# Kernel optimization log

Hardware: AMD Instinct MI355X
Metric: run time of the kernel (lower is better)

## Reference

```python
import jax, jax.numpy as jnp
import numpy as np

N, E, D, H, EF = 50000, 800000, 64, 64, 16


def setup_inputs() -> dict:
    key = jax.random.key(0)
    ks = jax.random.split(key, 12)
    s = 0.05
    return {
        "node_feat": jax.random.normal(ks[0], (N, D), jnp.float32),
        "coord": jax.random.normal(ks[1], (N, 3), jnp.float32),
        "edge_feat": jax.random.normal(ks[2], (E, EF), jnp.float32),
        "src": jax.random.randint(ks[3], (E,), 0, N, jnp.int32),
        "dst": jax.random.randint(ks[4], (E,), 0, N, jnp.int32),
        "W_e1": jax.random.normal(ks[5], (2 * D + EF + 1, H), jnp.float32) * s,
        "b_e1": jnp.zeros((H,), jnp.float32),
        "W_e2": jax.random.normal(ks[6], (H, H), jnp.float32) * s,
        "b_e2": jnp.zeros((H,), jnp.float32),
        "W_n1": jax.random.normal(ks[7], (D + H, H), jnp.float32) * s,
        "b_n1": jnp.zeros((H,), jnp.float32),
        "W_n2": jax.random.normal(ks[8], (H, D), jnp.float32) * s,
        "b_n2": jnp.zeros((D,), jnp.float32),
    }


def reference(node_feat, coord, edge_feat, src, dst,
              W_e1, b_e1, W_e2, b_e2, W_n1, b_n1, W_n2, b_n2):
    # per-edge radial distance: ||coord_src - coord_dst||^2  -> [E,1]
    x_diff = coord[src] - coord[dst]
    radial = jnp.sum(x_diff * x_diff, axis=-1, keepdims=True)
    # edge message MLP: concat [h_src, h_dst, radial, a] -> SiLU MLP
    f = jnp.concatenate([node_feat[src], node_feat[dst], radial, edge_feat], axis=-1)
    m = jax.nn.silu(f @ W_e1 + b_e1)
    msg = jax.nn.silu(m @ W_e2 + b_e2)  # [E,H]
    # scatter-sum aggregation to destination nodes
    h_neigh = jax.ops.segment_sum(msg, dst, num_segments=node_feat.shape[0])
    # node update MLP
    z = jnp.concatenate([node_feat, h_neigh], axis=-1)
    h = jax.nn.silu(z @ W_n1 + b_n1) @ W_n2 + b_n2
    return h
```

## Files before the change

### kernel.cpp

```cpp
#include <hip/hip_runtime.h>

#define D 64
#define H 64
#define EFD 16
#define MS 68
#define TE 128
#define TN 128
#define DPB 16

__device__ __forceinline__ float silu(float x) {
    return x / (1.0f + __expf(-x));
}

#define GEMM_STEP(acc_, a_, bf_) do { \
    const float* bp_ = (const float*)(bf_); \
    acc_[0] += (a_).x*bp_[0] + (a_).y*bp_[4] + (a_).z*bp_[8]  + (a_).w*bp_[12]; \
    acc_[1] += (a_).x*bp_[1] + (a_).y*bp_[5] + (a_).z*bp_[9]  + (a_).w*bp_[13]; \
    acc_[2] += (a_).x*bp_[2] + (a_).y*bp_[6] + (a_).z*bp_[10] + (a_).w*bp_[14]; \
    acc_[3] += (a_).x*bp_[3] + (a_).y*bp_[7] + (a_).z*bp_[11] + (a_).w*bp_[15]; \
} while (0)

#define PGEMM64(acc_, Wp_, wrow0_, eg_, hg_, smem_) do { \
    for (int k4 = 0; k4 < 16; k4++) { \
        float4 bf_[4]; \
        _Pragma("unroll") \
        for (int kk = 0; kk < 4; kk++) \
            bf_[kk] = *(const float4*)&(Wp_)[(size_t)((wrow0_) + 4*k4 + kk) * H + 4*(hg_)]; \
        _Pragma("unroll") \
        for (int i = 0; i < 8; i++) { \
            float4 a_ = *(const float4*)&(smem_)[(8*(eg_) + i) * MS + 4*k4]; \
            GEMM_STEP(acc_[i], a_, bf_); \
        } \
    } \
} while (0)


__global__ __launch_bounds__(256) void hist_kernel(
    const int* __restrict__ dst, int* __restrict__ deg, int E)
{
    int e = blockIdx.x * 256 + threadIdx.x;
    if (e < E) atomicAdd(&deg[dst[e]], 1);
}

__global__ __launch_bounds__(1024, 1) void scan_kernel(
    const int* __restrict__ deg, int* __restrict__ cursor, int N)
{
    __shared__ int wsums[16];
    __shared__ int carry_s;
    const int tid = threadIdx.x;
    const int lane = tid & 63, wid = tid >> 6;
    if (tid == 0) carry_s = 0;
    __syncthreads();
    for (int base = 0; base < N; base += 1024) {
        int idx = base + tid;
        int v = (idx < N) ? deg[idx] : 0;
        int x = v;
        #pragma unroll
        for (int off = 1; off < 64; off <<= 1) {
            int y = __shfl_up(x, off, 64);
            if (lane >= off) x += y;
        }
        if (lane == 63) wsums[wid] = x;
        __syncthreads();
        if (wid == 0) {
            int ws = (lane < 16) ? wsums[lane] : 0;
            #pragma unroll
            for (int off = 1; off < 16; off <<= 1) {
                int y = __shfl_up(ws, off, 64);
                if (lane >= off) ws += y;
            }
            if (lane < 16) wsums[lane] = ws;
        }
        __syncthreads();
        int wprefix = (wid > 0) ? wsums[wid - 1] : 0;
        int excl = carry_s + wprefix + x - v;
        if (idx < N) cursor[idx] = excl;
        __syncthreads();
        if (tid == 0) carry_s += wsums[15];
        __syncthreads();
    }
}

__global__ __launch_bounds__(256) void build2_kernel(
    const int* __restrict__ dst, const int* __restrict__ src,
    int* __restrict__ cursor,
    int* __restrict__ eidx, int* __restrict__ srcs, int* __restrict__ dsts,
    int E)
{
    int e = blockIdx.x * 256 + threadIdx.x;
    if (e < E) {
        int d2 = dst[e];
        int pos = atomicAdd(&cursor[d2], 1);
        eidx[pos] = e;
        srcs[pos] = src[e];
        dsts[pos] = d2;
    }
}

__global__ __launch_bounds__(256) void build_kernel(
    const int* __restrict__ dst, int* __restrict__ cursor,
    int* __restrict__ eidx, int E)
{
    int e = blockIdx.x * 256 + threadIdx.x;
    if (e < E) {
        int pos = atomicAdd(&cursor[dst[e]], 1);
        eidx[pos] = e;
    }
}


__global__ __launch_bounds__(256, 4) void pre_kernel(
    const float* __restrict__ node_feat,
    const float* __restrict__ W_e1, const float* __restrict__ b_e1,
    float* __restrict__ Pa, float* __restrict__ Pb, int N)
{
    __shared__ float smem[TN * MS];
    const int tid = threadIdx.x;
    const int nbase = blockIdx.x * TN;
    const int ng = tid >> 4, hg = tid & 15, k = tid & 63, no = tid >> 6;

    #pragma unroll
    for (int t = 0; t < 32; t++) {
        int gn = nbase + no + 4*t;
        int cg = (gn < N) ? gn : (N - 1);
        smem[(no + 4*t) * MS + k] = node_feat[(size_t)cg * D + k];
    }
    __syncthreads();

    float accA[8][4], accB[8][4];
    {
        float4 b0 = *(const float4*)&b_e1[4*hg];
        #pragma unroll
        for (int i = 0; i < 8; i++) {
            accA[i][0]=b0.x; accA[i][1]=b0.y; accA[i][2]=b0.z; accA[i][3]=b0.w;
            accB[i][0]=0.f;  accB[i][1]=0.f;  accB[i][2]=0.f;  accB[i][3]=0.f;
        }
    }
    PGEMM64(accA, W_e1, 0,  ng, hg, smem);
    PGEMM64(accB, W_e1, 64, ng, hg, smem);

    #pragma unroll
    for (int i = 0; i < 8; i++) {
        int gn = nbase + 8*ng + i;
        if (gn < N) {
            float4 a; a.x=accA[i][0]; a.y=accA[i][1]; a.z=accA[i][2]; a.w=accA[i][3];
            float4 b; b.x=accB[i][0]; b.y=accB[i][1]; b.z=accB[i][2]; b.w=accB[i][3];
            *(float4*)&Pa[(size_t)gn * H + 4*hg] = a;
            *(float4*)&Pb[(size_t)gn * H + 4*hg] = b;
        }
    }
}


__global__ __launch_bounds__(256, 4) void edge_kernel2(
    const float* __restrict__ Pa, const float* __restrict__ Pb,
    const float* __restrict__ coord,
    const float* __restrict__ edge_feat,
    const int* __restrict__ eidx, const int* __restrict__ srcs,
    const int* __restrict__ dsts,
    const int* __restrict__ cursor_end, const int* __restrict__ deg,
    const float* __restrict__ W_e1,
    const float* __restrict__ W_e2, const float* __restrict__ b_e2,
    float* __restrict__ h_neigh, int N)
{
    __shared__ float smem[TE * MS];
    __shared__ float hacc[DPB * H];
    __shared__ int ssrc[TE], sdlo[TE], seid[TE];

    const int tid = threadIdx.x;
    const int dst0 = blockIdx.x * DPB;
    const int dlast = min(dst0 + DPB, N) - 1;
    const int rs = cursor_end[dst0] - deg[dst0];
    const int re = cursor_end[dlast];

    for (int i = tid; i < DPB * H; i += 256) hacc[i] = 0.f;

    const int eg = tid >> 4;
    const int hg = tid & 15;

    for (int base = rs; base < re; base += TE) {
        const int cnt = min(re - base, TE);
        __syncthreads();

        if (tid < TE) {
            int e = 0, s = 0, dl = -1;
            float radial = 0.f;
            if (tid < cnt) {
                int p = base + tid;
                e = eidx[p]; s = srcs[p];
                int d2 = dsts[p]; dl = d2 - dst0;
                float dx = coord[s*3+0] - coord[d2*3+0];
                float dy = coord[s*3+1] - coord[d2*3+1];
                float dz = coord[s*3+2] - coord[d2*3+2];
                radial = dx*dx + dy*dy + dz*dz;
            }
            ssrc[tid] = s; sdlo[tid] = dl; seid[tid] = e;
            smem[tid * MS + 0] = radial;
        }
        __syncthreads();

        {
            const int k2 = tid & 15, e2 = tid >> 4;
            #pragma unroll
            for (int t = 0; t < 8; t++) {
                int r = e2 + 16*t;
                float v = (sdlo[r] >= 0) ? edge_feat[(size_t)seid[r] * EFD + k2] : 0.f;
                smem[r * MS + 1 + k2] = v;
            }
        }

        float acc[8][4];
        #pragma unroll
        for (int i = 0; i < 8; i++) {
            int r = 8*eg + i;
            int s = ssrc[r];
            int dl = sdlo[r];
            int drow = (dl >= 0) ? (dst0 + dl) : 0;
            float4 pa = *(const float4*)&Pa[(size_t)s * H + 4*hg];
            float4 pb = *(const float4*)&Pb[(size_t)drow * H + 4*hg];
            acc[i][0] = pa.x + pb.x; acc[i][1] = pa.y + pb.y;
            acc[i][2] = pa.z + pb.z; acc[i][3] = pa.w + pb.w;
        }
        __syncthreads();

        for (int k4 = 0; k4 < 4; k4++) {
            float4 bf[4];
            #pragma unroll
            for (int kk = 0; kk < 4; kk++)
                bf[kk] = *(const float4*)&W_e1[(size_t)(128 + 4*k4 + kk) * H + 4*hg];
            #pragma unroll
            for (int i = 0; i < 8; i++) {
                float4 a = *(const float4*)&smem[(8*eg + i) * MS + 4*k4];
                GEMM_STEP(acc[i], a, bf);
            }
        }
        {
            float4 b = *(const float4*)&W_e1[(size_t)144 * H + 4*hg];
            #pragma unroll
            for (int i = 0; i < 8; i++) {
                float a = smem[(8*eg+i)*MS + 16];
                acc[i][0] += a*b.x; acc[i][1] += a*b.y; acc[i][2] += a*b.z; acc[i][3] += a*b.w;
            }
        }
        __syncthreads();

        #pragma unroll
        for (int i = 0; i < 8; i++) {
            float4 mv;
            mv.x = silu(acc[i][0]); mv.y = silu(acc[i][1]);
            mv.z = silu(acc[i][2]); mv.w = silu(acc[i][3]);
            *(float4*)&smem[(8*eg+i)*MS + 4*hg] = mv;
        }
        __syncthreads();

        float acc2[8][4];
        {
            float4 b0 = *(const float4*)&b_e2[4*hg];
            #pragma unroll
            for (int i = 0; i < 8; i++) {
                acc2[i][0]=b0.x; acc2[i][1]=b0.y; acc2[i][2]=b0.z; acc2[i][3]=b0.w;
            }
        }
        PGEMM64(acc2, W_e2, 0, eg, hg, smem);

        float rx=0.f, ry=0.f, rz=0.f, rw=0.f;
        int cur = -1;
        #pragma unroll
        for (int i = 0; i < 8; i++) {
            int r = 8*eg + i;
            int dl = sdlo[r];
            if (dl < 0) continue;
            float vx = silu(acc2[i][0]), vy = silu(acc2[i][1]);
            float vz = silu(acc2[i][2]), vw = silu(acc2[i][3]);
            if (dl != cur) {
                if (cur >= 0) {
                    float* hp = &hacc[cur * H + 4*hg];
                    atomicAdd(&hp[0], rx); atomicAdd(&hp[1], ry);
                    atomicAdd(&hp[2], rz); atomicAdd(&hp[3], rw);
                }
                cur = dl; rx = vx; ry = vy; rz = vz; rw = vw;
            } else {
                rx += vx; ry += vy; rz += vz; rw += vw;
            }
        }
        if (cur >= 0) {
            float* hp = &hacc[cur * H + 4*hg];
            atomicAdd(&hp[0], rx); atomicAdd(&hp[1], ry);
            atomicAdd(&hp[2], rz); atomicAdd(&hp[3], rw);
        }
    }

    __syncthreads();
    {
        const int dloc = tid >> 4;
        const int ch = 4 * (tid & 15);
        int gd = dst0 + dloc;
        if (gd < N) {
            float4 v = *(const float4*)&hacc[dloc * H + ch];
            *(float4*)&h_neigh[(size_t)gd * H + ch] = v;
        }
    }
}


template <int MODE>
__global__ __launch_bounds__(256, 4) void edge_kernel(
    const float* __restrict__ node_feat,
    const float* __restrict__ coord,
    const float* __restrict__ edge_feat,
    const int* __restrict__ src,
    const int* __restrict__ dst,
    const int* __restrict__ eidx_g,
    const float* __restrict__ W_e1, const float* __restrict__ b_e1,
    const float* __restrict__ W_e2, const float* __restrict__ b_e2,
    float* __restrict__ h_neigh,
    int E)
{
    __shared__ float smem[TE * MS];
    __shared__ int ssrc[TE];
    __shared__ int sdst[TE];
    __shared__ int seid[TE];

    const int tid = threadIdx.x;
    const int ebase = blockIdx.x * TE;

    float radial = 0.f;
    if (tid < TE) {
        int p = ebase + tid;
        int e = p, s = 0, d2 = -1;
        if (p < E) {
            if (MODE == 1) e = eidx_g[p];
            s = src[e];
            d2 = dst[e];
        }
        ssrc[tid] = s;
        sdst[tid] = d2;
        seid[tid] = e;
        if (d2 >= 0) {
            float dx = coord[s*3+0] - coord[d2*3+0];
            float dy = coord[s*3+1] - coord[d2*3+1];
            float dz = coord[s*3+2] - coord[d2*3+2];
            radial = dx*dx + dy*dy + dz*dz;
        }
    }
    __syncthreads();

    const int eg = tid >> 4;
    const int hg = tid & 15;
    const int k  = tid & 63;
    const int eo = tid >> 6;

    float acc[8][4];
    {
        float4 b0 = *(const float4*)&b_e1[4*hg];
        #pragma unroll
        for (int i = 0; i < 8; i++) {
            acc[i][0]=b0.x; acc[i][1]=b0.y; acc[i][2]=b0.z; acc[i][3]=b0.w;
        }
    }

    float rA[32];
    #pragma unroll
    for (int t = 0; t < 32; t++)
        rA[t] = node_feat[(size_t)ssrc[eo + 4*t] * D + k];
    #pragma unroll
    for (int t = 0; t < 32; t++)
        smem[(eo + 4*t) * MS + k] = rA[t];
    __syncthreads();

    float rB[32];
    #pragma unroll
    for (int t = 0; t < 32; t++) {
        int row = sdst[eo + 4*t];
        row = row < 0 ? 0 : row;
        rB[t] = node_feat[(size_t)row * D + k];
    }
    PGEMM64(acc, W_e1, 0, eg, hg, smem);
    __syncthreads();

    #pragma unroll
    for (int t = 0; t < 32; t++)
        smem[(eo + 4*t) * MS + k] = rB[t];
    __syncthreads();

    float rC[8];
    {
        const int k2 = tid & 15, e2 = tid >> 4;
        #pragma unroll
        for (int t = 0; t < 8; t++) {
            int r = e2 + 16*t;
            rC[t] = (ebase + r < E) ? edge_feat[(size_t)seid[r] * EFD + k2] : 0.f;
        }
    }
    PGEMM64(acc, W_e1, 64, eg, hg, smem);
    __syncthreads();

    {
        const int k2 = tid & 15, e2 = tid >> 4;
        #pragma unroll
        for (int t = 0; t < 8; t++)
            smem[(e2 + 16*t) * MS + 1 + k2] = rC[t];
        if (tid < TE) smem[tid * MS + 0] = radial;
    }
    __syncthreads();

    for (int k4 = 0; k4 < 4; k4++) {
        float4 bf[4];
        #pragma unroll
        for (int kk = 0; kk < 4; kk++)
            bf[kk] = *(const float4*)&W_e1[(size_t)(128 + 4*k4 + kk) * H + 4*hg];
        #pragma unroll
        for (int i = 0; i < 8; i++) {
            float4 a = *(const float4*)&smem[(8*eg + i) * MS + 4*k4];
            GEMM_STEP(acc[i], a, bf);
        }
    }
    {
        float4 b = *(const float4*)&W_e1[(size_t)144 * H + 4*hg];
        #pragma unroll
        for (int i = 0; i < 8; i++) {
            float a = smem[(8*eg+i)*MS + 16];
            acc[i][0] += a*b.x; acc[i][1] += a*b.y; acc[i][2] += a*b.z; acc[i][3] += a*b.w;
        }
    }
    __syncthreads();

    #pragma unroll
    for (int i = 0; i < 8; i++) {
        float4 mv;
        mv.x = silu(acc[i][0]); mv.y = silu(acc[i][1]);
        mv.z = silu(acc[i][2]); mv.w = silu(acc[i][3]);
        *(float4*)&smem[(8*eg+i)*MS + 4*hg] = mv;
    }
    __syncthreads();

    float acc2[8][4];
    {
        float4 b0 = *(const float4*)&b_e2[4*hg];
        #pragma unroll
        for (int i = 0; i < 8; i++) {
            acc2[i][0]=b0.x; acc2[i][1]=b0.y; acc2[i][2]=b0.z; acc2[i][3]=b0.w;
        }
    }
    PGEMM64(acc2, W_e2, 0, eg, hg, smem);

    if (MODE == 0) {
        #pragma unroll
        for (int i = 0; i < 8; i++) {
            int r = 8*eg + i;
            int dr = sdst[r];
            if (dr >= 0) {
                float* hp = &h_neigh[(size_t)dr * H + 4*hg];
                atomicAdd(&hp[0], silu(acc2[i][0]));
                atomicAdd(&hp[1], silu(acc2[i][1]));
                atomicAdd(&hp[2], silu(acc2[i][2]));
                atomicAdd(&hp[3], silu(acc2[i][3]));
            }
        }
    } else {
        __syncthreads();
        #pragma unroll
        for (int i = 0; i < 8; i++) {
            float4 mv;
            mv.x = silu(acc2[i][0]); mv.y = silu(acc2[i][1]);
            mv.z = silu(acc2[i][2]); mv.w = silu(acc2[i][3]);
            *(float4*)&smem[(8*eg+i)*MS + 4*hg] = mv;
        }
        __syncthreads();

        int emaxt = E - ebase; if (emaxt > TE) emaxt = TE;
        #pragma unroll 1
        for (int i = 0; i < 8; i++) {
            int r = 8*eg + i;
            if (r >= emaxt) break;
            int dr = sdst[r];
            if (dr < 0) continue;
            if (r > 0 && sdst[r-1] == dr) continue;
            float4 s = *(const float4*)&smem[r*MS + 4*hg];
            int rr = r + 1;
            while (rr < emaxt && sdst[rr] == dr) {
                const float* mp = &smem[rr*MS + 4*hg];
                s.x += mp[0]; s.y += mp[1]; s.z += mp[2]; s.w += mp[3];
                rr++;
            }
            float* hp = &h_neigh[(size_t)dr * H + 4*hg];
            atomicAdd(&hp[0], s.x); atomicAdd(&hp[1], s.y);
            atomicAdd(&hp[2], s.z); atomicAdd(&hp[3], s.w);
        }
    }
}


__global__ __launch_bounds__(256, 4) void node_kernel(
    const float* __restrict__ node_feat,
    const float* __restrict__ h_neigh,
    const float* __restrict__ W_n1, const float* __restrict__ b_n1,
    const float* __restrict__ W_n2, const float* __restrict__ b_n2,
    float* __restrict__ out, int N)
{
    __shared__ float smem[TN * MS];

    const int tid = threadIdx.x;
    const int nbase = blockIdx.x * TN;

    const int ng = tid >> 4;
    const int hg = tid & 15;
    const int k  = tid & 63;
    const int no = tid >> 6;

    float acc[8][4];
    {
        float4 b0 = *(const float4*)&b_n1[4*hg];
        #pragma unroll
        for (int i = 0; i < 8; i++) {
            acc[i][0]=b0.x; acc[i][1]=b0.y; acc[i][2]=b0.z; acc[i][3]=b0.w;
        }
    }

    float rA[32];
    #pragma unroll
    for (int t = 0; t < 32; t++) {
        int gn = nbase + no + 4*t;
        int cg = (gn < N) ? gn : (N - 1);
        rA[t] = node_feat[(size_t)cg * D + k];
    }
    #pragma unroll
    for (int t = 0; t < 32; t++)
        smem[(no + 4*t) * MS + k] = rA[t];
    __syncthreads();

    float rB[32];
    #pragma unroll
    for (int t = 0; t < 32; t++) {
        int gn = nbase + no + 4*t;
        int cg = (gn < N) ? gn : (N - 1);
        rB[t] = h_neigh[(size_t)cg * H + k];
    }
    PGEMM64(acc, W_n1, 0, ng, hg, smem);
    __syncthreads();

    #pragma unroll
    for (int t = 0; t < 32; t++)
        smem[(no + 4*t) * MS + k] = rB[t];
    __syncthreads();

    PGEMM64(acc, W_n1, 64, ng, hg, smem);
    __syncthreads();

    #pragma unroll
    for (int i = 0; i < 8; i++) {
        float4 mv;
        mv.x = silu(acc[i][0]); mv.y = silu(acc[i][1]);
        mv.z = silu(acc[i][2]); mv.w = silu(acc[i][3]);
        *(float4*)&smem[(8*ng+i)*MS + 4*hg] = mv;
    }
    __syncthreads();

    float acc2[8][4];
    {
        float4 b0 = *(const float4*)&b_n2[4*hg];
        #pragma unroll
        for (int i = 0; i < 8; i++) {
            acc2[i][0]=b0.x; acc2[i][1]=b0.y; acc2[i][2]=b0.z; acc2[i][3]=b0.w;
        }
    }
    PGEMM64(acc2, W_n2, 0, ng, hg, smem);

    #pragma unroll
    for (int i = 0; i < 8; i++) {
        int gn = nbase + 8*ng + i;
        if (gn < N) {
            float4 ov;
            ov.x = acc2[i][0]; ov.y = acc2[i][1]; ov.z = acc2[i][2]; ov.w = acc2[i][3];
            *(float4*)&out[(size_t)gn * D + 4*hg] = ov;
        }
    }
}

extern "C" void kernel_launch(void* const* d_in, const int* in_sizes, int n_in,
                              void* d_out, int out_size, void* d_ws, size_t ws_size,
                              hipStream_t stream)
{
    const float* node_feat = (const float*)d_in[0];
    const float* coord     = (const float*)d_in[1];
    const float* edge_feat = (const float*)d_in[2];
    const int*   src       = (const int*)d_in[3];
    const int*   dst       = (const int*)d_in[4];
    const float* W_e1 = (const float*)d_in[5];
    const float* b_e1 = (const float*)d_in[6];
    const float* W_e2 = (const float*)d_in[7];
    const float* b_e2 = (const float*)d_in[8];
    const float* W_n1 = (const float*)d_in[9];
    const float* b_n1 = (const float*)d_in[10];
    const float* W_n2 = (const float*)d_in[11];
    const float* b_n2 = (const float*)d_in[12];

    const int N = in_sizes[0] / D;
    const int E = in_sizes[3];

    const size_t hn_b   = (size_t)N * H * sizeof(float);
    const size_t n_i    = (size_t)N * sizeof(int);
    const size_t e_i    = (size_t)E * sizeof(int);
    const size_t p_b    = (size_t)N * H * sizeof(float);

    const size_t need2 = hn_b + 2*n_i + 3*e_i + 2*p_b;
    const size_t need1 = hn_b + 2*n_i + e_i;

    float* h_neigh = (float*)d_ws;
    const int eblocks = (E + TE - 1) / TE;

    if (ws_size >= need2) {
        char* p = (char*)d_ws + hn_b;
        int* deg    = (int*)p;              p += n_i;
        int* cursor = (int*)p;              p += n_i;
        int* eidx   = (int*)p;              p += e_i;
        int* srcs   = (int*)p;              p += e_i;
        int* dsts   = (int*)p;              p += e_i;
        float* Pa   = (float*)p;            p += p_b;
        float* Pb   = (float*)p;

        hipMemsetAsync(deg, 0, n_i, stream);
        hist_kernel<<<(E + 255) / 256, 256, 0, stream>>>(dst, deg, E);
        scan_kernel<<<1, 1024, 0, stream>>>(deg, cursor, N);
        build2_kernel<<<(E + 255) / 256, 256, 0, stream>>>(dst, src, cursor,
                                                           eidx, srcs, dsts, E);
        pre_kernel<<<(N + TN - 1) / TN, 256, 0, stream>>>(node_feat, W_e1, b_e1,
                                                          Pa, Pb, N);
        const int dblocks = (N + DPB - 1) / DPB;
        edge_kernel2<<<dblocks, 256, 0, stream>>>(Pa, Pb, coord, edge_feat,
                                                  eidx, srcs, dsts, cursor, deg,
                                                  W_e1, W_e2, b_e2, h_neigh, N);
    } else if (ws_size >= need1) {
        int* deg    = (int*)((char*)d_ws + hn_b);
        int* cursor = (int*)((char*)deg + n_i);
        int* eidx   = (int*)((char*)cursor + n_i);
        hipMemsetAsync(d_ws, 0, hn_b + n_i, stream);
        hist_kernel<<<(E + 255) / 256, 256, 0, stream>>>(dst, deg, E);
        scan_kernel<<<1, 1024, 0, stream>>>(deg, cursor, N);
        build_kernel<<<(E + 255) / 256, 256, 0, stream>>>(dst, cursor, eidx, E);
        edge_kernel<1><<<eblocks, 256, 0, stream>>>(node_feat, coord, edge_feat,
                                                    src, dst, eidx,
                                                    W_e1, b_e1, W_e2, b_e2,
                                                    h_neigh, E);
    } else {
        hipMemsetAsync(d_ws, 0, hn_b, stream);
        edge_kernel<0><<<eblocks, 256, 0, stream>>>(node_feat, coord, edge_feat,
                                                    src, dst, nullptr,
                                                    W_e1, b_e1, W_e2, b_e2,
                                                    h_neigh, E);
    }

    const int nblocks = (N + TN - 1) / TN;
    node_kernel<<<nblocks, 256, 0, stream>>>(node_feat, h_neigh,
                                             W_n1, b_n1, W_n2, b_n2,
                                             (float*)d_out, N);
}
```

Baseline: 646.8 us.

## Parallelize degree scan, pre-sort edge features with radial, prefetch next edge tile

Replaces the single-block serial scan with a three-kernel block-partitioned scan (reduce, scan partials, apply). The build step now writes edge features and the precomputed radial into a CSR-ordered 20-float record per edge, so the edge kernel reads them contiguously instead of gathering through eidx and coord. The new edge kernel reads these records directly from global memory, and it issues the Pa/Pb gathers for the next tile before the second GEMM to overlap latency. The cost is an extra E*80-byte buffer written and read, a larger workspace requirement, and higher register pressure (occupancy hint lowered to 3).

```diff
diff --git a/kernel.cpp b/kernel.cpp
--- a/kernel.cpp
+++ b/kernel.cpp
@@ -7,6 +7,7 @@
 #define TE 128
 #define TN 128
 #define DPB 16
+#define REFW 20
 
 __device__ __forceinline__ float silu(float x) {
     return x / (1.0f + __expf(-x));
@@ -42,43 +43,96 @@
     if (e < E) atomicAdd(&deg[dst[e]], 1);
 }
 
-__global__ __launch_bounds__(1024, 1) void scan_kernel(
-    const int* __restrict__ deg, int* __restrict__ cursor, int N)
-{
-    __shared__ int wsums[16];
+
+__global__ __launch_bounds__(256) void scanA_kernel(
+    const int* __restrict__ deg, int* __restrict__ part, int N)
+{
+    __shared__ int tmp[256];
+    const int tid = threadIdx.x;
+    int idx = blockIdx.x * 256 + tid;
+    tmp[tid] = (idx < N) ? deg[idx] : 0;
+    __syncthreads();
+    for (int off = 128; off > 0; off >>= 1) {
+        if (tid < off) tmp[tid] += tmp[tid + off];
+        __syncthreads();
+    }
+    if (tid == 0) part[blockIdx.x] = tmp[0];
+}
+
+__global__ __launch_bounds__(256, 1) void scanB_kernel(
+    int* __restrict__ part, int nparts)
+{
+    __shared__ int tmp[256];
     __shared__ int carry_s;
     const int tid = threadIdx.x;
-    const int lane = tid & 63, wid = tid >> 6;
     if (tid == 0) carry_s = 0;
     __syncthreads();
-    for (int base = 0; base < N; base += 1024) {
+    for (int base = 0; base < nparts; base += 256) {
         int idx = base + tid;
-        int v = (idx < N) ? deg[idx] : 0;
-        int x = v;
-        #pragma unroll
-        for (int off = 1; off < 64; off <<= 1) {
-            int y = __shfl_up(x, off, 64);
-            if (lane >= off) x += y;
-        }
-        if (lane == 63) wsums[wid] = x;
-        __syncthreads();
-        if (wid == 0) {
-            int ws = (lane < 16) ? wsums[lane] : 0;
-            #pragma unroll
-            for (int off = 1; off < 16; off <<= 1) {
-                int y = __shfl_up(ws, off, 64);
-                if (lane >= off) ws += y;
-            }
-            if (lane < 16) wsums[lane] = ws;
-        }
-        __syncthreads();
-        int wprefix = (wid > 0) ? wsums[wid - 1] : 0;
-        int excl = carry_s + wprefix + x - v;
-        if (idx < N) cursor[idx] = excl;
-        __syncthreads();
-        if (tid == 0) carry_s += wsums[15];
-        __syncthreads();
-    }
+        int v = (idx < nparts) ? part[idx] : 0;
+        tmp[tid] = v;
+        __syncthreads();
+        #pragma unroll
+        for (int off = 1; off < 256; off <<= 1) {
+            int t = (tid >= off) ? tmp[tid - off] : 0;
+            __syncthreads();
+            tmp[tid] += t;
+            __syncthreads();
+        }
+        int incl = tmp[tid];
+        int tot = tmp[255];
+        if (idx < nparts) part[idx] = carry_s + incl - v;
+        __syncthreads();
+        if (tid == 0) carry_s += tot;
+        __syncthreads();
+    }
+}
+
+__global__ __launch_bounds__(256) void scanC_kernel(
+    const int* __restrict__ deg, const int* __restrict__ part,
+    int* __restrict__ cursor, int N)
+{
+    __shared__ int tmp[256];
+    const int tid = threadIdx.x;
+    int idx = blockIdx.x * 256 + tid;
+    int v = (idx < N) ? deg[idx] : 0;
+    tmp[tid] = v;
+    __syncthreads();
+    #pragma unroll
+    for (int off = 1; off < 256; off <<= 1) {
+        int t = (tid >= off) ? tmp[tid - off] : 0;
+        __syncthreads();
+        tmp[tid] += t;
+        __syncthreads();
+    }
+    if (idx < N) cursor[idx] = part[blockIdx.x] + tmp[tid] - v;
+}
+
+
+__global__ __launch_bounds__(256) void build3_kernel(
+    const int* __restrict__ dst, const int* __restrict__ src,
+    const float* __restrict__ coord, const float* __restrict__ edge_feat,
+    int* __restrict__ cursor,
+    int* __restrict__ srcs, int* __restrict__ dsts, float* __restrict__ refr,
+    int E)
+{
+    int e = blockIdx.x * 256 + threadIdx.x;
+    if (e >= E) return;
+    int d2 = dst[e];
+    int s = src[e];
+    int pos = atomicAdd(&cursor[d2], 1);
+    srcs[pos] = s;
+    dsts[pos] = d2;
+    float dx = coord[s*3+0] - coord[d2*3+0];
+    float dy = coord[s*3+1] - coord[d2*3+1];
+    float dz = coord[s*3+2] - coord[d2*3+2];
+    float* rr = &refr[(size_t)pos * REFW];
+    const float4* ef = (const float4*)&edge_feat[(size_t)e * EFD];
+    *(float4*)&rr[0]  = ef[0];
+    *(float4*)&rr[4]  = ef[1];
+    *(float4*)&rr[8]  = ef[2];
+    *(float4*)&rr[12] = ef[3];
+    rr[16] = dx*dx + dy*dy + dz*dz;
 }
 
 __global__ __launch_bounds__(256) void build2_kernel(
@@ -97,17 +151,6 @@
     }
 }
 
-__global__ __launch_bounds__(256) void build_kernel(
-    const int* __restrict__ dst, int* __restrict__ cursor,
-    int* __restrict__ eidx, int E)
-{
-    int e = blockIdx.x * 256 + threadIdx.x;
-    if (e < E) {
-        int pos = atomicAdd(&cursor[dst[e]], 1);
-        eidx[pos] = e;
-    }
-}
-
 
 __global__ __launch_bounds__(256, 4) void pre_kernel(
     const float* __restrict__ node_feat,
@@ -149,6 +192,147 @@
             *(float4*)&Pb[(size_t)gn * H + 4*hg] = b;
         }
     }
+}
+
+
+__global__ __launch_bounds__(256, 3) void edge_kernel3(
+    const float* __restrict__ Pa, const float* __restrict__ Pb,
+    const int* __restrict__ srcs, const int* __restrict__ dsts,
+    const float* __restrict__ refr,
+    const int* __restrict__ cursor_end, const int* __restrict__ deg,
+    const float* __restrict__ W_e1,
+    const float* __restrict__ W_e2, const float* __restrict__ b_e2,
+    float* __restrict__ h_neigh, int N)
+{
+    __shared__ float smem[TE * MS];
+    __shared__ float hacc[DPB * H];
+
+    const int tid = threadIdx.x;
+    const int dst0 = blockIdx.x * DPB;
+    const int dlast = min(dst0 + DPB, N) - 1;
+    const int rs = cursor_end[dst0] - deg[dst0];
+    const int re = cursor_end[dlast];
+
+    for (int i = tid; i < DPB * H; i += 256) hacc[i] = 0.f;
+
+    const int eg = tid >> 4, hg = tid & 15;
+
+    float acc[8][4];
+    int dl[8];
+
+    #define LOAD_TILE(base_, acc_, dl_) do { \
+        _Pragma("unroll") \
+        for (int i_ = 0; i_ < 8; i_++) { \
+            int p_ = (base_) + 8*eg + i_; \
+            bool val_ = (p_ < re); \
+            int pp_ = val_ ? p_ : (re - 1); \
+            int s_ = srcs[pp_]; \
+            int d2_ = dsts[pp_]; \
+            float4 pa_ = *(const float4*)&Pa[(size_t)s_ * H + 4*hg]; \
+            float4 pb_ = *(const float4*)&Pb[(size_t)d2_ * H + 4*hg]; \
+            acc_[i_][0] = pa_.x + pb_.x; acc_[i_][1] = pa_.y + pb_.y; \
+            acc_[i_][2] = pa_.z + pb_.z; acc_[i_][3] = pa_.w + pb_.w; \
+            dl_[i_] = val_ ? (d2_ - dst0) : -1; \
+        } \
+    } while (0)
+
+    if (re > rs) LOAD_TILE(rs, acc, dl);
+
+    for (int base = rs; base < re; base += TE) {
+        for (int k4 = 0; k4 < 4; k4++) {
+            float4 bf[4];
+            #pragma unroll
+            for (int kk = 0; kk < 4; kk++)
+                bf[kk] = *(const float4*)&W_e1[(size_t)(129 + 4*k4 + kk) * H + 4*hg];
+            #pragma unroll
+            for (int i = 0; i < 8; i++) {
+                int p = base + 8*eg + i;
+                int pp = (p < re) ? p : (re - 1);
+                float4 a = *(const float4*)&refr[(size_t)pp * REFW + 4*k4];
+                GEMM_STEP(acc[i], a, bf);
+            }
+        }
+        {
+            float4 b = *(const float4*)&W_e1[(size_t)128 * H + 4*hg];
+            #pragma unroll
+            for (int i = 0; i < 8; i++) {
+                int p = base + 8*eg + i;
+                int pp = (p < re) ? p : (re - 1);
+                float a = refr[(size_t)pp * REFW + 16];
+                acc[i][0] += a*b.x; acc[i][1] += a*b.y;
+                acc[i][2] += a*b.z; acc[i][3] += a*b.w;
+            }
+        }
+
+        #pragma unroll
+        for (int i = 0; i < 8; i++) {
+            float4 mv;
+            mv.x = silu(acc[i][0]); mv.y = silu(acc[i][1]);
+            mv.z = silu(acc[i][2]); mv.w = silu(acc[i][3]);
+            *(float4*)&smem[(8*eg+i)*MS + 4*hg] = mv;
+        }
+
+        float nacc[8][4]; int ndl[8];
+        const int nb = base + TE;
+        if (nb < re) LOAD_TILE(nb, nacc, ndl);
+
+        __syncthreads();
+
+        float acc2[8][4];
+        {
+            float4 b0 = *(const float4*)&b_e2[4*hg];
+            #pragma unroll
+            for (int i = 0; i < 8; i++) {
+                acc2[i][0]=b0.x; acc2[i][1]=b0.y; acc2[i][2]=b0.z; acc2[i][3]=b0.w;
+            }
+        }
+        PGEMM64(acc2, W_e2, 0, eg, hg, smem);
+
+        float rx=0.f, ry=0.f, rz=0.f, rw=0.f;
+        int cur = -1;
+        #pragma unroll
+        for (int i = 0; i < 8; i++) {
+            int d = dl[i];
+            if (d < 0) continue;
+            float vx = silu(acc2[i][0]), vy = silu(acc2[i][1]);
+            float vz = silu(acc2[i][2]), vw = silu(acc2[i][3]);
+            if (d != cur) {
+                if (cur >= 0) {
+                    float* hp = &hacc[cur * H + 4*hg];
+                    atomicAdd(&hp[0], rx); atomicAdd(&hp[1], ry);
+                    atomicAdd(&hp[2], rz); atomicAdd(&hp[3], rw);
+                }
+                cur = d; rx = vx; ry = vy; rz = vz; rw = vw;
+            } else {
+                rx += vx; ry += vy; rz += vz; rw += vw;
+            }
+        }
+        if (cur >= 0) {
+            float* hp = &hacc[cur * H + 4*hg];
+            atomicAdd(&hp[0], rx); atomicAdd(&hp[1], ry);
+            atomicAdd(&hp[2], rz); atomicAdd(&hp[3], rw);
+        }
+
+        __syncthreads();
+
+        #pragma unroll
+        for (int i = 0; i < 8; i++) {
+            acc[i][0]=nacc[i][0]; acc[i][1]=nacc[i][1];
+            acc[i][2]=nacc[i][2]; acc[i][3]=nacc[i][3];
+            dl[i]=ndl[i];
+        }
+    }
+
+    __syncthreads();
+    {
+        const int dloc = tid >> 4, ch = 4 * (tid & 15);
+        int gd = dst0 + dloc;
+        if (gd < N) {
+            float4 v = *(const float4*)&hacc[dloc * H + ch];
+            *(float4*)&h_neigh[(size_t)gd * H + ch] = v;
+        }
+    }
+    #undef LOAD_TILE
 }
 
 
@@ -175,26 +359,25 @@
 
     for (int i = tid; i < DPB * H; i += 256) hacc[i] = 0.f;
 
-    const int eg = tid >> 4;
-    const int hg = tid & 15;
+    const int eg = tid >> 4, hg = tid & 15;
 
     for (int base = rs; base < re; base += TE) {
         const int cnt = min(re - base, TE);
         __syncthreads();
 
         if (tid < TE) {
-            int e = 0, s = 0, dl = -1;
+            int e = 0, s = 0, dlv = -1;
             float radial = 0.f;
             if (tid < cnt) {
                 int p = base + tid;
                 e = eidx[p]; s = srcs[p];
-                int d2 = dsts[p]; dl = d2 - dst0;
+                int d2 = dsts[p]; dlv = d2 - dst0;
                 float dx = coord[s*3+0] - coord[d2*3+0];
                 float dy = coord[s*3+1] - coord[d2*3+1];
                 float dz = coord[s*3+2] - coord[d2*3+2];
                 radial = dx*dx + dy*dy + dz*dz;
             }
-            ssrc[tid] = s; sdlo[tid] = dl; seid[tid] = e;
+            ssrc[tid] = s; sdlo[tid] = dlv; seid[tid] = e;
             smem[tid * MS + 0] = radial;
         }
         __syncthreads();
@@ -214,8 +397,8 @@
         for (int i = 0; i < 8; i++) {
             int r = 8*eg + i;
             int s = ssrc[r];
-            int dl = sdlo[r];
-            int drow = (dl >= 0) ? (dst0 + dl) : 0;
+            int dlv = sdlo[r];
+            int drow = (dlv >= 0) ? (dst0 + dlv) : 0;
             float4 pa = *(const float4*)&Pa[(size_t)s * H + 4*hg];
             float4 pb = *(const float4*)&Pb[(size_t)drow * H + 4*hg];
             acc[i][0] = pa.x + pb.x; acc[i][1] = pa.y + pb.y;
@@ -268,17 +451,17 @@
         #pragma unroll
         for (int i = 0; i < 8; i++) {
             int r = 8*eg + i;
-            int dl = sdlo[r];
-            if (dl < 0) continue;
+            int dlv = sdlo[r];
+            if (dlv < 0) continue;
             float vx = silu(acc2[i][0]), vy = silu(acc2[i][1]);
             float vz = silu(acc2[i][2]), vw = silu(acc2[i][3]);
-            if (dl != cur) {
+            if (dlv != cur) {
                 if (cur >= 0) {
                     float* hp = &hacc[cur * H + 4*hg];
                     atomicAdd(&hp[0], rx); atomicAdd(&hp[1], ry);
                     atomicAdd(&hp[2], rz); atomicAdd(&hp[3], rw);
                 }
-                cur = dl; rx = vx; ry = vy; rz = vz; rw = vw;
+                cur = dlv; rx = vx; ry = vy; rz = vz; rw = vw;
             } else {
                 rx += vx; ry += vy; rz += vz; rw += vw;
             }
@@ -292,200 +475,11 @@
 
     __syncthreads();
     {
-        const int dloc = tid >> 4;
-        const int ch = 4 * (tid & 15);
+        const int dloc = tid >> 4, ch = 4 * (tid & 15);
         int gd = dst0 + dloc;
         if (gd < N) {
             float4 v = *(const float4*)&hacc[dloc * H + ch];
             *(float4*)&h_neigh[(size_t)gd * H + ch] = v;
-        }
-    }
-}
-
-
-template <int MODE>
-__global__ __launch_bounds__(256, 4) void edge_kernel(
-    const float* __restrict__ node_feat,
-    const float* __restrict__ coord,
-    const float* __restrict__ edge_feat,
-    const int* __restrict__ src,
-    const int* __restrict__ dst,
-    const int* __restrict__ eidx_g,
-    const float* __restrict__ W_e1, const float* __restrict__ b_e1,
-    const float* __restrict__ W_e2, const float* __restrict__ b_e2,
-    float* __restrict__ h_neigh,
-    int E)
-{
-    __shared__ float smem[TE * MS];
-    __shared__ int ssrc[TE];
-    __shared__ int sdst[TE];
-    __shared__ int seid[TE];
-
-    const int tid = threadIdx.x;
-    const int ebase = blockIdx.x * TE;
-
-    float radial = 0.f;
-    if (tid < TE) {
-        int p = ebase + tid;
-        int e = p, s = 0, d2 = -1;
-        if (p < E) {
-            if (MODE == 1) e = eidx_g[p];
-            s = src[e];
-            d2 = dst[e];
-        }
-        ssrc[tid] = s;
-        sdst[tid] = d2;
-        seid[tid] = e;
-        if (d2 >= 0) {
-            float dx = coord[s*3+0] - coord[d2*3+0];
-            float dy = coord[s*3+1] - coord[d2*3+1];
-            float dz = coord[s*3+2] - coord[d2*3+2];
-            radial = dx*dx + dy*dy + dz*dz;
-        }
-    }
-    __syncthreads();
-
-    const int eg = tid >> 4;
-    const int hg = tid & 15;
-    const int k  = tid & 63;
-    const int eo = tid >> 6;
-
-    float acc[8][4];
-    {
-        float4 b0 = *(const float4*)&b_e1[4*hg];
-        #pragma unroll
-        for (int i = 0; i < 8; i++) {
-            acc[i][0]=b0.x; acc[i][1]=b0.y; acc[i][2]=b0.z; acc[i][3]=b0.w;
-        }
-    }
-
-    float rA[32];
-    #pragma unroll
-    for (int t = 0; t < 32; t++)
-        rA[t] = node_feat[(size_t)ssrc[eo + 4*t] * D + k];
-    #pragma unroll
-    for (int t = 0; t < 32; t++)
-        smem[(eo + 4*t) * MS + k] = rA[t];
-    __syncthreads();
-
-    float rB[32];
-    #pragma unroll
-    for (int t = 0; t < 32; t++) {
-        int row = sdst[eo + 4*t];
-        row = row < 0 ? 0 : row;
-        rB[t] = node_feat[(size_t)row * D + k];
-    }
-    PGEMM64(acc, W_e1, 0, eg, hg, smem);
-    __syncthreads();
-
-    #pragma unroll
-    for (int t = 0; t < 32; t++)
-        smem[(eo + 4*t) * MS + k] = rB[t];
-    __syncthreads();
-
-    float rC[8];
-    {
-        const int k2 = tid & 15, e2 = tid >> 4;
-        #pragma unroll
-        for (int t = 0; t < 8; t++) {
-            int r = e2 + 16*t;
-            rC[t] = (ebase + r < E) ? edge_feat[(size_t)seid[r] * EFD + k2] : 0.f;
-        }
-    }
-    PGEMM64(acc, W_e1, 64, eg, hg, smem);
-    __syncthreads();
-
-    {
-        const int k2 = tid & 15, e2 = tid >> 4;
-        #pragma unroll
-        for (int t = 0; t < 8; t++)
-            smem[(e2 + 16*t) * MS + 1 + k2] = rC[t];
-        if (tid < TE) smem[tid * MS + 0] = radial;
-    }
-    __syncthreads();
-
-    for (int k4 = 0; k4 < 4; k4++) {
-        float4 bf[4];
-        #pragma unroll
-        for (int kk = 0; kk < 4; kk++)
-            bf[kk] = *(const float4*)&W_e1[(size_t)(128 + 4*k4 + kk) * H + 4*hg];
-        #pragma unroll
-        for (int i = 0; i < 8; i++) {
-            float4 a = *(const float4*)&smem[(8*eg + i) * MS + 4*k4];
-            GEMM_STEP(acc[i], a, bf);
-        }
-    }
-    {
-        float4 b = *(const float4*)&W_e1[(size_t)144 * H + 4*hg];
-        #pragma unroll
-        for (int i = 0; i < 8; i++) {
-            float a = smem[(8*eg+i)*MS + 16];
-            acc[i][0] += a*b.x; acc[i][1] += a*b.y; acc[i][2] += a*b.z; acc[i][3] += a*b.w;
-        }
-    }
-    __syncthreads();
-
-    #pragma unroll
-    for (int i = 0; i < 8; i++) {
-        float4 mv;
-        mv.x = silu(acc[i][0]); mv.y = silu(acc[i][1]);
-        mv.z = silu(acc[i][2]); mv.w = silu(acc[i][3]);
-        *(float4*)&smem[(8*eg+i)*MS + 4*hg] = mv;
-    }
-    __syncthreads();
-
-    float acc2[8][4];
-    {
-        float4 b0 = *(const float4*)&b_e2[4*hg];
-        #pragma unroll
-        for (int i = 0; i < 8; i++) {
-            acc2[i][0]=b0.x; acc2[i][1]=b0.y; acc2[i][2]=b0.z; acc2[i][3]=b0.w;
-        }
-    }
-    PGEMM64(acc2, W_e2, 0, eg, hg, smem);
-
-    if (MODE == 0) {
-        #pragma unroll
-        for (int i = 0; i < 8; i++) {
-            int r = 8*eg + i;
-            int dr = sdst[r];
-            if (dr >= 0) {
-                float* hp = &h_neigh[(size_t)dr * H + 4*hg];
-                atomicAdd(&hp[0], silu(acc2[i][0]));
-                atomicAdd(&hp[1], silu(acc2[i][1]));
-                atomicAdd(&hp[2], silu(acc2[i][2]));
-                atomicAdd(&hp[3], silu(acc2[i][3]));
-            }
-        }
-    } else {
-        __syncthreads();
-        #pragma unroll
-        for (int i = 0; i < 8; i++) {
-            float4 mv;
-            mv.x = silu(acc2[i][0]); mv.y = silu(acc2[i][1]);
-            mv.z = silu(acc2[i][2]); mv.w = silu(acc2[i][3]);
-            *(float4*)&smem[(8*eg+i)*MS + 4*hg] = mv;
-        }
-        __syncthreads();
-
-        int emaxt = E - ebase; if (emaxt > TE) emaxt = TE;
-        #pragma unroll 1
-        for (int i = 0; i < 8; i++) {
-            int r = 8*eg + i;
-            if (r >= emaxt) break;
-            int dr = sdst[r];
-            if (dr < 0) continue;
-            if (r > 0 && sdst[r-1] == dr) continue;
-            float4 s = *(const float4*)&smem[r*MS + 4*hg];
-            int rr = r + 1;
-            while (rr < emaxt && sdst[rr] == dr) {
-                const float* mp = &smem[rr*MS + 4*hg];
-                s.x += mp[0]; s.y += mp[1]; s.z += mp[2]; s.w += mp[3];
-                rr++;
-            }
-            float* hp = &h_neigh[(size_t)dr * H + 4*hg];
-            atomicAdd(&hp[0], s.x); atomicAdd(&hp[1], s.y);
-            atomicAdd(&hp[2], s.z); atomicAdd(&hp[3], s.w);
         }
     }
 }
@@ -503,10 +497,7 @@
     const int tid = threadIdx.x;
     const int nbase = blockIdx.x * TN;
 
-    const int ng = tid >> 4;
-    const int hg = tid & 15;
-    const int k  = tid & 63;
-    const int no = tid >> 6;
+    const int ng = tid >> 4, hg = tid & 15, k = tid & 63, no = tid >> 6;
 
     float acc[8][4];
     {
@@ -597,57 +588,67 @@
 
     const int N = in_sizes[0] / D;
     const int E = in_sizes[3];
-
-    const size_t hn_b   = (size_t)N * H * sizeof(float);
-    const size_t n_i    = (size_t)N * sizeof(int);
-    const size_t e_i    = (size_t)E * sizeof(int);
-    const size_t p_b    = (size_t)N * H * sizeof(float);
-
-    const size_t need2 = hn_b + 2*n_i + 3*e_i + 2*p_b;
-    const size_t need1 = hn_b + 2*n_i + e_i;
+    const int NP = (N + 255) / 256;
+
+    const size_t hn_b  = (size_t)N * H * sizeof(float);
+    const size_t n_i   = (size_t)N * sizeof(int);
+    const size_t e_i   = (size_t)E * sizeof(int);
+    const size_t pt_b  = 1024 * sizeof(int);
+    const size_t p_b   = (size_t)N * H * sizeof(float);
+    const size_t rf_b  = (size_t)E * REFW * sizeof(float);
+
+    const size_t need3 = hn_b + 2*n_i + pt_b + 2*e_i + rf_b + 2*p_b;
+    const size_t need2 = hn_b + 2*n_i + pt_b + 3*e_i + 2*p_b;
 
     float* h_neigh = (float*)d_ws;
-    const int eblocks = (E + TE - 1) / TE;
-
-    if (ws_size >= need2) {
+    const int dblocks = (N + DPB - 1) / DPB;
+
+    if (ws_size >= need3) {
         char* p = (char*)d_ws + hn_b;
-        int* deg    = (int*)p;              p += n_i;
-        int* cursor = (int*)p;              p += n_i;
-        int* eidx   = (int*)p;              p += e_i;
-        int* srcs   = (int*)p;              p += e_i;
-        int* dsts   = (int*)p;              p += e_i;
-        float* Pa   = (float*)p;            p += p_b;
+        int* deg    = (int*)p;   p += n_i;
+        int* cursor = (int*)p;   p += n_i;
+        int* part   = (int*)p;   p += pt_b;
+        int* srcs   = (int*)p;   p += e_i;
+        int* dsts   = (int*)p;   p += e_i;
+        float* refr = (float*)p; p += rf_b;
+        float* Pa   = (float*)p; p += p_b;
         float* Pb   = (float*)p;
 
         hipMemsetAsync(deg, 0, n_i, stream);
         hist_kernel<<<(E + 255) / 256, 256, 0, stream>>>(dst, deg, E);
-        scan_kernel<<<1, 1024, 0, stream>>>(deg, cursor, N);
+        scanA_kernel<<<NP, 256, 0, stream>>>(deg, part, N);
+        scanB_kernel<<<1, 256, 0, stream>>>(part, NP);
+        scanC_kernel<<<NP, 256, 0, stream>>>(deg, part, cursor, N);
+        build3_kernel<<<(E + 255) / 256, 256, 0, stream>>>(dst, src, coord, edge_feat,
+                                                           cursor, srcs, dsts, refr, E);
+        pre_kernel<<<(N + TN - 1) / TN, 256, 0, stream>>>(node_feat, W_e1, b_e1,
+                                                          Pa, Pb, N);
+        edge_kernel3<<<dblocks, 256, 0, stream>>>(Pa, Pb, srcs, dsts, refr,
+                                                  cursor, deg,
+                                                  W_e1, W_e2, b_e2, h_neigh, N);
+    } else {
+        char* p = (char*)d_ws + hn_b;
+        int* deg    = (int*)p;   p += n_i;
+        int* cursor = (int*)p;   p += n_i;
+        int* part   = (int*)p;   p += pt_b;
+        int* eidx   = (int*)p;   p += e_i;
+        int* srcs   = (int*)p;   p += e_i;
+        int* dsts   = (int*)p;   p += e_i;
+        float* Pa   = (float*)p; p += p_b;
+        float* Pb   = (float*)p;
+
+        hipMemsetAsync(deg, 0, n_i, stream);
+        hist_kernel<<<(E + 255) / 256, 256, 0, stream>>>(dst, deg, E);
+        scanA_kernel<<<NP, 256, 0, stream>>>(deg, part, N);
+        scanB_kernel<<<1, 256, 0, stream>>>(part, NP);
+        scanC_kernel<<<NP, 256, 0, stream>>>(deg, part, cursor, N);
         build2_kernel<<<(E + 255) / 256, 256, 0, stream>>>(dst, src, cursor,
                                                            eidx, srcs, dsts, E);
         pre_kernel<<<(N + TN - 1) / TN, 256, 0, stream>>>(node_feat, W_e1, b_e1,
                                                           Pa, Pb, N);
-        const int dblocks = (N + DPB - 1) / DPB;
         edge_kernel2<<<dblocks, 256, 0, stream>>>(Pa, Pb, coord, edge_feat,
                                                   eidx, srcs, dsts, cursor, deg,
                                                   W_e1, W_e2, b_e2, h_neigh, N);
-    } else if (ws_size >= need1) {
-        int* deg    = (int*)((char*)d_ws + hn_b);
-        int* cursor = (int*)((char*)deg + n_i);
-        int* eidx   = (int*)((char*)cursor + n_i);
-        hipMemsetAsync(d_ws, 0, hn_b + n_i, stream);
-        hist_kernel<<<(E + 255) / 256, 256, 0, stream>>>(dst, deg, E);
-        scan_kernel<<<1, 1024, 0, stream>>>(deg, cursor, N);
-        build_kernel<<<(E + 255) / 256, 256, 0, stream>>>(dst, cursor, eidx, E);
-        edge_kernel<1><<<eblocks, 256, 0, stream>>>(node_feat, coord, edge_feat,
-                                                    src, dst, eidx,
-                                                    W_e1, b_e1, W_e2, b_e2,
-                                                    h_neigh, E);
-    } else {
-        hipMemsetAsync(d_ws, 0, hn_b, stream);
-        edge_kernel<0><<<eblocks, 256, 0, stream>>>(node_feat, coord, edge_feat,
-                                                    src, dst, nullptr,
-                                                    W_e1, b_e1, W_e2, b_e2,
-                                                    h_neigh, E);
     }
 
     const int nblocks = (N + TN - 1) / TN;
```

Result: faster. 610.4 us (-5.6%).
